# Kernel optimization log

Measured on AMD Instinct MI355X. Metric: run time of the kernel, lower is better.

The kernel has to match this reference:

```python
import jax, jax.numpy as jnp
import numpy as np

H, DH = 16, 64            # heads, dim_head (rope dim == DH)
NUM_CHAINS = 2
TWO_PI = 2.0 * np.pi
LN_EPS = 1e-5


def layer_norm(x, gamma):
    mu = jnp.mean(x, axis=-1, keepdims=True)
    var = jnp.var(x, axis=-1, keepdims=True)
    return (x - mu) * jax.lax.rsqrt(var + LN_EPS) * gamma


def rotate_half(x):
    # pairs are interleaved: (..., d*2) viewed as (..., d, 2); (x1,x2)->(-x2,x1)
    x1 = x[..., 0::2]
    x2 = x[..., 1::2]
    return jnp.stack((-x2, x1), axis=-1).reshape(x.shape)


def cyclic_rope_freqs(residue_index, chain_index, cyclic_mask, rope_freqs, dtype):
    """Angles [B,L,DH]: standard RoPE (with chain-offset combination) for linear
    tokens, ring harmonics omega_i = 2*pi*k_i/L_chain for cyclic tokens."""
    t = residue_index.astype(dtype)                      # B L (interpolate_factor=1)
    ci = chain_index.astype(dtype)
    F = rope_freqs.shape[0]                              # DH//2 = 32
    # standard path (RotaryEmbedding._forward with chain_index):
    # residue_indices = arange(F)%F = identity; chain_indices = arange(F)//F = 0
    res = t[..., None] * rope_freqs                      # B L F
    ch0 = ci * rope_freqs[0]                             # B L  (chain_freqs[...,0])
    std = jnp.repeat(res + ch0[..., None], 2, axis=-1)   # B L DH (interleaved repeat)
    # ring size per token: count of cyclic tokens on each token's chain
    oh = jax.nn.one_hot(chain_index, NUM_CHAINS, dtype=dtype)        # B L C
    counts = jnp.einsum('blc,bl->bc', oh, cyclic_mask)               # B C
    ring = jnp.take_along_axis(counts, chain_index, axis=1) * cyclic_mask  # B L
    ring_safe = jnp.maximum(ring, 1.0)
    max_k = jnp.maximum(jnp.floor(ring_safe * 0.5), 1.0)             # B L
    kk = jnp.arange(1, F + 1, dtype=dtype)
    k_eff = jnp.where(max_k[..., None] == 1.0, 1.0,
                      1.0 + jnp.mod(kk - 1.0, max_k[..., None]))     # B L F
    omega = TWO_PI * k_eff / ring_safe[..., None]                    # B L F
    cyc = jnp.repeat(omega * t[..., None], 2, axis=-1)               # B L DH
    return jnp.where((cyclic_mask > 0)[..., None], cyc, std)


def setup_inputs() -> dict:
    key = jax.random.key(0)
    ks = jax.random.split(key, 8)
    B, L, dim = 4, 1024, 1024
    s = 0.02
    x = jax.random.normal(ks[0], (B, L, dim), jnp.float32)
    time = jax.random.normal(ks[1], (B, 1, dim), jnp.float32)
    seq_mask = jnp.ones((B, L), jnp.float32)
    residue_index = (jnp.arange(B * L, dtype=jnp.int32).reshape(B, L)) % L
    chain_index = jax.random.randint(ks[2], (B, L), 0, NUM_CHAINS).astype(jnp.int32)
    cyclic_mask = jax.random.randint(ks[3], (B, L), 0, 2).astype(jnp.float32)
    gamma = jnp.ones((dim,), jnp.float32)
    Wt = jax.random.normal(ks[4], (2 * dim, dim), jnp.float32) * s
    bt = jnp.zeros((2 * dim,), jnp.float32)
    Wq = jax.random.normal(ks[5], (H * DH, dim), jnp.float32) * s
    Wkv = jax.random.normal(ks[6], (2 * H * DH, dim), jnp.float32) * s
    Wo = jax.random.normal(ks[7], (dim, H * DH), jnp.float32) * s
    rope_freqs = 1.0 / (10000.0 ** (jnp.arange(0, DH, 2, dtype=jnp.float32) / DH))
    return {"x": x, "time": time, "seq_mask": seq_mask, "cyclic_mask": cyclic_mask,
            "gamma": gamma, "Wt": Wt, "bt": bt, "Wq": Wq, "Wkv": Wkv, "Wo": Wo,
            "rope_freqs": rope_freqs,
            "residue_index": residue_index, "chain_index": chain_index}


def reference(x, time, seq_mask, cyclic_mask, gamma, Wt, bt, Wq, Wkv, Wo,
              rope_freqs, residue_index, chain_index):
    B, L, dim = x.shape
    x = x * seq_mask[..., None]
    xn = layer_norm(x, gamma)
    # time conditioning: SiLU -> Linear -> (scale, shift)
    ss = jax.nn.silu(time) @ Wt.T + bt                   # B 1 2*dim
    scale, shift = jnp.split(ss, 2, axis=-1)
    xc = xn * (scale + 1.0) + shift                      # B L dim
    q = (xc @ Wq.T).reshape(B, L, H, DH).transpose(0, 2, 1, 3)   # B H L Dh
    k, v = jnp.split(xc @ Wkv.T, 2, axis=-1)
    k = k.reshape(B, L, H, DH).transpose(0, 2, 1, 3)
    v = v.reshape(B, L, H, DH).transpose(0, 2, 1, 3)
    # cyclic rotary embeddings (full head dim rotated)
    freqs = cyclic_rope_freqs(residue_index, chain_index, cyclic_mask,
                              rope_freqs, x.dtype)        # B L DH
    cos_f = jnp.cos(freqs)[:, None]                       # B 1 L DH
    sin_f = jnp.sin(freqs)[:, None]
    q = q * cos_f + rotate_half(q) * sin_f
    k = k * cos_f + rotate_half(k) * sin_f
    sim = jnp.einsum('bhid,bhjd->bhij', q * (DH ** -0.5), k)
    neg = -jnp.finfo(sim.dtype).max
    sim = jnp.where(seq_mask[:, None, None, :] > 0, sim, neg)
    attn = jax.nn.softmax(sim, axis=-1)
    out = jnp.einsum('bhij,bhjd->bhid', attn, v)
    out = out.transpose(0, 2, 1, 3).reshape(B, L, H * DH)
    out = out @ Wo.T
    return out * seq_mask[..., None]
```

## Files before the change

kernel.cpp:

```cpp
#include <hip/hip_runtime.h>
#include <math.h>

#define NB 4
#define NL 1024
#define NDIM 1024
#define NH 16
#define NDH 64
#define NEG_MAX (-3.402823466e38f)

typedef __attribute__((ext_vector_type(4))) float fx4;
typedef __attribute__((ext_vector_type(8))) short bh8;

__device__ __forceinline__ ushort f2bf(float f){
    unsigned u = __float_as_uint(f);
    u += 0x7fff + ((u>>16)&1);
    return (ushort)(u>>16);
}
__device__ __forceinline__ float bf2f(ushort h){
    return __uint_as_float(((unsigned)h)<<16);
}
__device__ __forceinline__ void gload16(const void* g, void* l){
    __builtin_amdgcn_global_load_lds((const __attribute__((address_space(1))) void*)g,
                                     (__attribute__((address_space(3))) void*)l, 16, 0, 0);
}

__global__ __launch_bounds__(256) void k_silu(const float* __restrict__ t, float* __restrict__ o){
    int i = blockIdx.x*256 + threadIdx.x;
    float v = t[i];
    o[i] = v / (1.f + __expf(-v));
}

__global__ __launch_bounds__(256) void k_ss(const float* __restrict__ st, const float* __restrict__ Wt,
                                            const float* __restrict__ bt, float* __restrict__ ss){
    int gw   = (blockIdx.x*256 + threadIdx.x) >> 6;
    int lane = threadIdx.x & 63;
    int b = gw >> 11, j = gw & 2047;
    const float* a = st + b*NDIM;
    const float* w = Wt + (size_t)j*NDIM;
    float s = 0.f;
    #pragma unroll 4
    for (int i = lane; i < NDIM; i += 64) s += a[i]*w[i];
    #pragma unroll
    for (int off=32; off; off>>=1) s += __shfl_xor(s, off, 64);
    if (!lane) ss[gw] = s + bt[j];
}

__global__ __launch_bounds__(256) void k_counts(const int* __restrict__ chain, const float* __restrict__ cyc,
                                                float* __restrict__ counts){
    int b = blockIdx.x >> 1, c = blockIdx.x & 1;
    float s = 0.f;
    for (int l = threadIdx.x; l < NL; l += 256)
        s += (chain[b*NL+l]==c) ? cyc[b*NL+l] : 0.f;
    __shared__ float red[4];
    #pragma unroll
    for (int off=32; off; off>>=1) s += __shfl_xor(s, off, 64);
    if (!(threadIdx.x & 63)) red[threadIdx.x>>6] = s;
    __syncthreads();
    if (!threadIdx.x) counts[blockIdx.x] = red[0]+red[1]+red[2]+red[3];
}

__global__ __launch_bounds__(256) void k_angles(const int* __restrict__ resi, const int* __restrict__ chain,
                                                const float* __restrict__ cyc, const float* __restrict__ rf,
                                                const float* __restrict__ counts,
                                                float* __restrict__ cosb, float* __restrict__ sinb){
    int idx = blockIdx.x*256 + threadIdx.x;
    int f  = idx & 31;
    int bl = idx >> 5;
    int b  = bl >> 10;
    float t  = (float)resi[bl];
    int   ci = chain[bl];
    float cm = cyc[bl];
    float ang;
    if (cm > 0.f) {
        float ring      = counts[b*2+ci] * cm;
        float ring_safe = fmaxf(ring, 1.f);
        float max_k     = fmaxf(floorf(ring_safe*0.5f), 1.f);
        float k_eff     = (max_k == 1.f) ? 1.f : (1.f + fmodf((float)f, max_k));
        float omega     = 6.28318530717958647692f * k_eff / ring_safe;
        ang = omega * t;
    } else {
        ang = t * rf[f] + (float)ci * rf[0];
    }
    cosb[idx] = cosf(ang);
    sinb[idx] = sinf(ang);
}

__global__ __launch_bounds__(256) void k_conv(const float* __restrict__ s, ushort* __restrict__ d){
    int i = (blockIdx.x*256 + threadIdx.x)*4;
    fx4 v = *(const fx4*)(s+i);
    ushort4 o; o.x=f2bf(v.x); o.y=f2bf(v.y); o.z=f2bf(v.z); o.w=f2bf(v.w);
    *(ushort4*)(d+i) = o;
}

__global__ __launch_bounds__(256) void k_lnmod(const float* __restrict__ x, const float* __restrict__ sm,
                                               const float* __restrict__ gamma, const float* __restrict__ ss,
                                               ushort* __restrict__ xc){
    int row = blockIdx.x;
    int b   = row >> 10;
    int t   = threadIdx.x;
    float msk = sm[row];
    fx4 v = ((const fx4*)(x + (size_t)row*NDIM))[t];
    v.x*=msk; v.y*=msk; v.z*=msk; v.w*=msk;
    float s1 = v.x+v.y+v.z+v.w;
    float s2 = v.x*v.x + v.y*v.y + v.z*v.z + v.w*v.w;
    __shared__ float r1[4], r2[4];
    #pragma unroll
    for (int off=32; off; off>>=1){ s1 += __shfl_xor(s1,off,64); s2 += __shfl_xor(s2,off,64); }
    if (!(t & 63)){ r1[t>>6]=s1; r2[t>>6]=s2; }
    __syncthreads();
    s1 = r1[0]+r1[1]+r1[2]+r1[3];
    s2 = r2[0]+r2[1]+r2[2]+r2[3];
    float mu  = s1 * (1.f/NDIM);
    float var = s2 * (1.f/NDIM) - mu*mu;
    float rs  = rsqrtf(var + 1e-5f);
    const float* sc = ss + b*2048;
    fx4 g   = ((const fx4*)gamma)[t];
    fx4 scl = ((const fx4*)sc)[t];
    fx4 sh  = ((const fx4*)(sc+1024))[t];
    ushort4 ob;
    ob.x = f2bf((v.x-mu)*rs*g.x*(1.f+scl.x)+sh.x);
    ob.y = f2bf((v.y-mu)*rs*g.y*(1.f+scl.y)+sh.y);
    ob.z = f2bf((v.z-mu)*rs*g.z*(1.f+scl.z)+sh.z);
    ob.w = f2bf((v.w-mu)*rs*g.w*(1.f+scl.w)+sh.w);
    *(ushort4*)(xc + (size_t)row*NDIM + t*4) = ob;
}

template<int MODE>
__global__ __launch_bounds__(256) void k_mm(const ushort* __restrict__ A, const ushort* __restrict__ W,
                                            ushort* __restrict__ qo, ushort* __restrict__ ko,
                                            ushort* __restrict__ vo,
                                            float* __restrict__ outf, const float* __restrict__ smask){
    __shared__ ushort As[128*32];
    __shared__ ushort Bs[128*32];
    int t = threadIdx.x, l = t&63, w = t>>6;
    int lo = l&15, hi = l>>4;
    int m0 = blockIdx.y*128, n0 = blockIdx.x*128;
    int wm = (w>>1)*64, wn = (w&1)*64;
    fx4 acc[4][4];
    #pragma unroll
    for (int i=0;i<4;i++)
        #pragma unroll
        for (int j=0;j<4;j++) acc[i][j] = (fx4){0.f,0.f,0.f,0.f};
    const char* Ab = (const char*)A;
    const char* Wb = (const char*)W;
    for (int k0=0; k0<NDIM; k0+=32){
        __syncthreads();
        #pragma unroll
        for (int e=0;e<2;e++){
            int c = t + e*256;
            int row = c>>2, cw = c&3;
            gload16(Ab + (size_t)(m0+row)*2048 + k0*2 + cw*16, (char*)As + c*16);
            gload16(Wb + (size_t)(n0+row)*2048 + k0*2 + cw*16, (char*)Bs + c*16);
        }
        __syncthreads();
        bh8 af[4], bf[4];
        #pragma unroll
        for (int i=0;i<4;i++) af[i] = *(const bh8*)(As + (wm + i*16 + lo)*32 + hi*8);
        #pragma unroll
        for (int j=0;j<4;j++) bf[j] = *(const bh8*)(Bs + (wn + j*16 + lo)*32 + hi*8);
        #pragma unroll
        for (int i=0;i<4;i++)
            #pragma unroll
            for (int j=0;j<4;j++)
                acc[i][j] = __builtin_amdgcn_mfma_f32_16x16x32_bf16(af[i], bf[j], acc[i][j], 0, 0, 0);
    }
    #pragma unroll
    for (int i=0;i<4;i++){
        #pragma unroll
        for (int r=0;r<4;r++){
            int m = m0 + wm + i*16 + hi*4 + r;
            int b_ = m>>10, l_ = m&1023;
            #pragma unroll
            for (int j=0;j<4;j++){
                int n = n0 + wn + j*16 + lo;
                float val = acc[i][j][r];
                if (MODE==0){
                    int nn = n & 1023;
                    int h_ = nn>>6, d_ = nn&63;
                    size_t off = (size_t)((b_*NH + h_)*NL + l_)*NDH + d_;
                    if (n < 1024)      qo[off] = f2bf(val);
                    else if (n < 2048) ko[off] = f2bf(val);
                    else               vo[off] = f2bf(val);
                } else {
                    outf[(size_t)m*NDIM + n] = val * smask[m];
                }
            }
        }
    }
}

__global__ __launch_bounds__(256) void k_rope(ushort* __restrict__ q, ushort* __restrict__ k,
                                              const float* __restrict__ cosb, const float* __restrict__ sinb){
    int idx = blockIdx.x*256 + threadIdx.x;
    int f   = idx & 31;
    int bhl = idx >> 5;
    int l   = bhl & 1023;
    int b   = bhl >> 14;
    int ca  = ((b<<10)|l)*32 + f;
    float c = cosb[ca], s = sinb[ca];
    unsigned qp = ((const unsigned*)q)[idx];
    unsigned kp = ((const unsigned*)k)[idx];
    float qx = bf2f((ushort)(qp&0xffffu)), qy = bf2f((ushort)(qp>>16));
    float kx = bf2f((ushort)(kp&0xffffu)), ky = bf2f((ushort)(kp>>16));
    float q0 = (qx*c - qy*s)*0.125f, q1 = (qy*c + qx*s)*0.125f;
    float k0 = kx*c - ky*s,          k1 = ky*c + kx*s;
    ((unsigned*)q)[idx] = (unsigned)f2bf(q0) | ((unsigned)f2bf(q1)<<16);
    ((unsigned*)k)[idx] = (unsigned)f2bf(k0) | ((unsigned)f2bf(k1)<<16);
}

__global__ __launch_bounds__(256) void k_vt(const ushort* __restrict__ v, ushort* __restrict__ vt){
    __shared__ ushort tile[64][65];
    int t = threadIdx.x;
    int bh = blockIdx.y, l0 = blockIdx.x*64;
    #pragma unroll
    for (int e=0;e<2;e++){
        int c = t + e*256;
        int row = c>>3, cw = c&7;
        bh8 d = *(const bh8*)(v + ((size_t)bh*NL + l0 + row)*NDH + cw*8);
        #pragma unroll
        for (int x=0;x<8;x++) tile[row][cw*8+x] = (ushort)d[x];
    }
    __syncthreads();
    #pragma unroll
    for (int e=0;e<2;e++){
        int c = t + e*256;
        int drow = c>>3, cw = c&7;
        bh8 o;
        #pragma unroll
        for (int x=0;x<8;x++) o[x] = (short)tile[cw*8+x][drow];
        *(bh8*)(vt + ((size_t)bh*NDH + drow)*NL + l0 + cw*8) = o;
    }
}

__global__ __launch_bounds__(256) void k_fattn(const ushort* __restrict__ qb, const ushort* __restrict__ kb,
                                               const ushort* __restrict__ vt, const float* __restrict__ smask,
                                               ushort* __restrict__ ao){
    __shared__ ushort Ks[64*64];
    __shared__ ushort Vs[64*64];
    __shared__ ushort Ps[4][16*64];
    __shared__ float  smt[64];
    int t = threadIdx.x, l = t&63, w = t>>6;
    int bh = blockIdx.y, b = bh>>4, h = bh&15;
    int q0 = blockIdx.x*64;
    int lo = l&15, hi = l>>4;

    const ushort* qrowp = qb + ((size_t)bh*NL + q0 + w*16 + lo)*NDH;
    bh8 aq0 = *(const bh8*)(qrowp + hi*8);
    bh8 aq1 = *(const bh8*)(qrowp + 32 + hi*8);

    fx4 o[4];
    float mrun[4], lrun[4];
    #pragma unroll
    for (int d=0;d<4;d++) o[d] = (fx4){0.f,0.f,0.f,0.f};
    #pragma unroll
    for (int r=0;r<4;r++){ mrun[r]=NEG_MAX; lrun[r]=0.f; }

    const char* kbase = (const char*)(kb + (size_t)bh*NL*NDH);
    const char* vbase = (const char*)(vt + (size_t)bh*NDH*NL);
    char* KsB = (char*)Ks;
    char* VsB = (char*)Vs;
    char* PsB = (char*)&Ps[w][0];

    for (int j0=0; j0<NL; j0+=64){
        __syncthreads();
        #pragma unroll
        for (int e=0;e<2;e++){
            int c = t + e*256;
            int row = c>>3, cw = c&7;
            int lc = cw ^ (row&7);
            gload16(kbase + (size_t)(j0+row)*128 + lc*16, KsB + c*16);
            gload16(vbase + (size_t)row*2048 + j0*2 + lc*16, VsB + c*16);
        }
        if (t < 64) smt[t] = smask[b*NL + j0 + t];
        __syncthreads();

        fx4 s[4];
        #pragma unroll
        for (int j=0;j<4;j++){
            int row = j*16 + lo;
            int swz = (row&7)<<4;
            bh8 bk0 = *(const bh8*)(KsB + row*128 + ((hi*16) ^ swz));
            bh8 bk1 = *(const bh8*)(KsB + row*128 + ((64 + hi*16) ^ swz));
            fx4 z = (fx4){0.f,0.f,0.f,0.f};
            z = __builtin_amdgcn_mfma_f32_16x16x32_bf16(aq0, bk0, z, 0,0,0);
            z = __builtin_amdgcn_mfma_f32_16x16x32_bf16(aq1, bk1, z, 0,0,0);
            float msk = smt[row];
            s[j] = (msk > 0.f) ? z : (fx4){NEG_MAX,NEG_MAX,NEG_MAX,NEG_MAX};
        }

        float p[4][4];
        #pragma unroll
        for (int r=0;r<4;r++){
            float mt = fmaxf(fmaxf(s[0][r],s[1][r]), fmaxf(s[2][r],s[3][r]));
            #pragma unroll
            for (int off=1; off<16; off<<=1) mt = fmaxf(mt, __shfl_xor(mt, off));
            float mnew = fmaxf(mrun[r], mt);
            float cc = __expf(mrun[r]-mnew);
            float rs = 0.f;
            #pragma unroll
            for (int j=0;j<4;j++){ p[j][r] = __expf(s[j][r]-mnew); rs += p[j][r]; }
            #pragma unroll
            for (int off=1; off<16; off<<=1) rs += __shfl_xor(rs, off);
            lrun[r] = lrun[r]*cc + rs;
            mrun[r] = mnew;
            #pragma unroll
            for (int d=0;d<4;d++) o[d][r] *= cc;
        }

        #pragma unroll
        for (int r=0;r<4;r++){
            int qr = hi*4 + r;
            int swz = (qr&7)<<4;
            #pragma unroll
            for (int j=0;j<4;j++){
                int kv = j*16 + lo;
                *(ushort*)(PsB + qr*128 + ((kv*2) ^ swz)) = f2bf(p[j][r]);
            }
        }
        int swq = (lo&7)<<4;
        bh8 ap0 = *(const bh8*)(PsB + lo*128 + ((hi*16) ^ swq));
        bh8 ap1 = *(const bh8*)(PsB + lo*128 + ((64 + hi*16) ^ swq));

        #pragma unroll
        for (int d=0;d<4;d++){
            int row = d*16 + lo;
            int swz = (row&7)<<4;
            bh8 bv0 = *(const bh8*)(VsB + row*128 + ((hi*16) ^ swz));
            bh8 bv1 = *(const bh8*)(VsB + row*128 + ((64 + hi*16) ^ swz));
            o[d] = __builtin_amdgcn_mfma_f32_16x16x32_bf16(ap0, bv0, o[d], 0,0,0);
            o[d] = __builtin_amdgcn_mfma_f32_16x16x32_bf16(ap1, bv1, o[d], 0,0,0);
        }
    }

    #pragma unroll
    for (int r=0;r<4;r++){
        float inv = 1.f / lrun[r];
        int l_ = q0 + w*16 + hi*4 + r;
        size_t base = ((size_t)b*NL + l_)*NDIM + h*NDH;
        #pragma unroll
        for (int d=0;d<4;d++)
            ao[base + d*16 + lo] = f2bf(o[d][r]*inv);
    }
}

extern "C" void kernel_launch(void* const* d_in, const int* in_sizes, int n_in,
                              void* d_out, int out_size, void* d_ws, size_t ws_size,
                              hipStream_t stream) {
    const float* x      = (const float*)d_in[0];
    const float* time_  = (const float*)d_in[1];
    const float* smask  = (const float*)d_in[2];
    const float* cycm   = (const float*)d_in[3];
    const float* gamma  = (const float*)d_in[4];
    const float* Wt     = (const float*)d_in[5];
    const float* bt     = (const float*)d_in[6];
    const float* Wq     = (const float*)d_in[7];
    const float* Wkv    = (const float*)d_in[8];
    const float* Wo     = (const float*)d_in[9];
    const float* rf     = (const float*)d_in[10];
    const int*   resi   = (const int*)d_in[11];
    const int*   chain  = (const int*)d_in[12];
    float* out = (float*)d_out;

    float*  silu_t = (float*)d_ws;
    float*  ss     = silu_t + 4096;
    float*  cnts   = ss + 8192;
    float*  cosb   = cnts + 16;
    float*  sinb   = cosb + 131072;
    ushort* xc     = (ushort*)(sinb + 131072);
    ushort* wqkv   = xc + 4194304;
    ushort* wo     = wqkv + 3145728;
    ushort* qbuf   = wo + 1048576;
    ushort* kbuf   = qbuf + 4194304;
    ushort* vbuf   = kbuf + 4194304;
    ushort* vtb    = vbuf + 4194304;
    ushort* aob    = vtb + 4194304;

    hipLaunchKernelGGL(k_silu,   dim3(16),        dim3(256), 0, stream, time_, silu_t);
    hipLaunchKernelGGL(k_ss,     dim3(2048),      dim3(256), 0, stream, silu_t, Wt, bt, ss);
    hipLaunchKernelGGL(k_counts, dim3(8),         dim3(256), 0, stream, chain, cycm, cnts);
    hipLaunchKernelGGL(k_angles, dim3(512),       dim3(256), 0, stream, resi, chain, cycm, rf, cnts, cosb, sinb);
    hipLaunchKernelGGL(k_conv,   dim3(1024),      dim3(256), 0, stream, Wq,  wqkv);
    hipLaunchKernelGGL(k_conv,   dim3(2048),      dim3(256), 0, stream, Wkv, wqkv + 1048576);
    hipLaunchKernelGGL(k_conv,   dim3(1024),      dim3(256), 0, stream, Wo,  wo);
    hipLaunchKernelGGL(k_lnmod,  dim3(4096),      dim3(256), 0, stream, x, smask, gamma, ss, xc);
    hipLaunchKernelGGL((k_mm<0>), dim3(24,32),    dim3(256), 0, stream, xc, wqkv, qbuf, kbuf, vbuf, (float*)nullptr, (const float*)nullptr);
    hipLaunchKernelGGL(k_rope,   dim3(8192),      dim3(256), 0, stream, qbuf, kbuf, cosb, sinb);
    hipLaunchKernelGGL(k_vt,     dim3(16,64),     dim3(256), 0, stream, vbuf, vtb);
    hipLaunchKernelGGL(k_fattn,  dim3(16,64),     dim3(256), 0, stream, qbuf, kbuf, vtb, smask, aob);
    hipLaunchKernelGGL((k_mm<1>), dim3(8,32),     dim3(256), 0, stream, aob, wo, (ushort*)nullptr, (ushort*)nullptr, (ushort*)nullptr, out, smask);
}
```

Measured before the change: 250.2 us.

## Restructure flash attention with double-buffered KV, 128-row tiles and exp2 softmax

```diff
diff --git a/kernel.cpp b/kernel.cpp
--- a/kernel.cpp
+++ b/kernel.cpp
@@ -1,4 +1,5 @@
 #include <hip/hip_runtime.h>
+#include <hip/hip_bf16.h>
 #include <math.h>
 
 #define NB 4
@@ -12,9 +13,8 @@
 typedef __attribute__((ext_vector_type(8))) short bh8;
 
 __device__ __forceinline__ ushort f2bf(float f){
-    unsigned u = __float_as_uint(f);
-    u += 0x7fff + ((u>>16)&1);
-    return (ushort)(u>>16);
+    __hip_bfloat16 h = __float2bfloat16(f);
+    return *(ushort*)&h;
 }
 __device__ __forceinline__ float bf2f(ushort h){
     return __uint_as_float(((unsigned)h)<<16);
@@ -24,22 +24,19 @@
                                      (__attribute__((address_space(3))) void*)l, 16, 0, 0);
 }
 
-__global__ __launch_bounds__(256) void k_silu(const float* __restrict__ t, float* __restrict__ o){
-    int i = blockIdx.x*256 + threadIdx.x;
-    float v = t[i];
-    o[i] = v / (1.f + __expf(-v));
-}
-
-__global__ __launch_bounds__(256) void k_ss(const float* __restrict__ st, const float* __restrict__ Wt,
+__global__ __launch_bounds__(256) void k_ss(const float* __restrict__ time_, const float* __restrict__ Wt,
                                             const float* __restrict__ bt, float* __restrict__ ss){
     int gw   = (blockIdx.x*256 + threadIdx.x) >> 6;
     int lane = threadIdx.x & 63;
     int b = gw >> 11, j = gw & 2047;
-    const float* a = st + b*NDIM;
+    const float* a = time_ + b*NDIM;
     const float* w = Wt + (size_t)j*NDIM;
     float s = 0.f;
     #pragma unroll 4
-    for (int i = lane; i < NDIM; i += 64) s += a[i]*w[i];
+    for (int i = lane; i < NDIM; i += 64){
+        float v = a[i];
+        s += (v / (1.f + __expf(-v))) * w[i];
+    }
     #pragma unroll
     for (int off=32; off; off>>=1) s += __shfl_xor(s, off, 64);
     if (!lane) ss[gw] = s + bt[j];
@@ -85,11 +82,22 @@
     sinb[idx] = sinf(ang);
 }
 
-__global__ __launch_bounds__(256) void k_conv(const float* __restrict__ s, ushort* __restrict__ d){
+__global__ __launch_bounds__(256) void k_convall(const float* __restrict__ Wq, const float* __restrict__ Wkv,
+                                                 const float* __restrict__ Wo,
+                                                 ushort* __restrict__ wqkv, ushort* __restrict__ wo){
     int i = (blockIdx.x*256 + threadIdx.x)*4;
-    fx4 v = *(const fx4*)(s+i);
+    if (i >= 4194304) return;
+    const float* src; ushort* dst;
+    if (i < 3145728){
+        dst = wqkv + i;
+        src = (i < 1048576) ? (Wq + i) : (Wkv + (i - 1048576));
+    } else {
+        dst = wo + (i - 3145728);
+        src = Wo + (i - 3145728);
+    }
+    fx4 v = *(const fx4*)src;
     ushort4 o; o.x=f2bf(v.x); o.y=f2bf(v.y); o.z=f2bf(v.z); o.w=f2bf(v.w);
-    *(ushort4*)(d+i) = o;
+    *(ushort4*)dst = o;
 }
 
 __global__ __launch_bounds__(256) void k_lnmod(const float* __restrict__ x, const float* __restrict__ sm,
@@ -198,12 +206,13 @@
     int b   = bhl >> 14;
     int ca  = ((b<<10)|l)*32 + f;
     float c = cosb[ca], s = sinb[ca];
+    const float QS = 0.18033688011112042f;
     unsigned qp = ((const unsigned*)q)[idx];
     unsigned kp = ((const unsigned*)k)[idx];
     float qx = bf2f((ushort)(qp&0xffffu)), qy = bf2f((ushort)(qp>>16));
     float kx = bf2f((ushort)(kp&0xffffu)), ky = bf2f((ushort)(kp>>16));
-    float q0 = (qx*c - qy*s)*0.125f, q1 = (qy*c + qx*s)*0.125f;
-    float k0 = kx*c - ky*s,          k1 = ky*c + kx*s;
+    float q0 = (qx*c - qy*s)*QS, q1 = (qy*c + qx*s)*QS;
+    float k0 = kx*c - ky*s,      k1 = ky*c + kx*s;
     ((unsigned*)q)[idx] = (unsigned)f2bf(q0) | ((unsigned)f2bf(q1)<<16);
     ((unsigned*)k)[idx] = (unsigned)f2bf(k0) | ((unsigned)f2bf(k1)<<16);
 }
@@ -235,111 +244,164 @@
 __global__ __launch_bounds__(256) void k_fattn(const ushort* __restrict__ qb, const ushort* __restrict__ kb,
                                                const ushort* __restrict__ vt, const float* __restrict__ smask,
                                                ushort* __restrict__ ao){
-    __shared__ ushort Ks[64*64];
-    __shared__ ushort Vs[64*64];
-    __shared__ ushort Ps[4][16*64];
-    __shared__ float  smt[64];
+    __shared__ ushort Ks[2][64*64];
+    __shared__ ushort Vs[2][64*64];
+    __shared__ ushort Ps[4][32*64];
     int t = threadIdx.x, l = t&63, w = t>>6;
-    int bh = blockIdx.y, b = bh>>4, h = bh&15;
-    int q0 = blockIdx.x*64;
     int lo = l&15, hi = l>>4;
-
-    const ushort* qrowp = qb + ((size_t)bh*NL + q0 + w*16 + lo)*NDH;
-    bh8 aq0 = *(const bh8*)(qrowp + hi*8);
-    bh8 aq1 = *(const bh8*)(qrowp + 32 + hi*8);
-
-    fx4 o[4];
-    float mrun[4], lrun[4];
-    #pragma unroll
-    for (int d=0;d<4;d++) o[d] = (fx4){0.f,0.f,0.f,0.f};
-    #pragma unroll
-    for (int r=0;r<4;r++){ mrun[r]=NEG_MAX; lrun[r]=0.f; }
+    int logical = (blockIdx.x & 7)*64 + (blockIdx.x >> 3);
+    int bh = logical >> 3;
+    int qt = logical & 7;
+    int b = bh>>4, h = bh&15;
+    int q0 = qt*128;
+    int swzq = (lo&7)<<4;
+
+    bh8 aq[2][2];
+    #pragma unroll
+    for (int qs=0; qs<2; qs++){
+        const ushort* qrow = qb + ((size_t)bh*NL + q0 + w*32 + qs*16 + lo)*NDH;
+        aq[qs][0] = *(const bh8*)(qrow + hi*8);
+        aq[qs][1] = *(const bh8*)(qrow + 32 + hi*8);
+    }
+    const float* mrow = smask + b*NL;
+
+    fx4 o[2][4];
+    float mrun[2], lrun[2];
+    #pragma unroll
+    for (int qs=0; qs<2; qs++){
+        mrun[qs]=NEG_MAX; lrun[qs]=0.f;
+        #pragma unroll
+        for (int dt=0; dt<4; dt++) o[qs][dt] = (fx4){0.f,0.f,0.f,0.f};
+    }
 
     const char* kbase = (const char*)(kb + (size_t)bh*NL*NDH);
     const char* vbase = (const char*)(vt + (size_t)bh*NDH*NL);
-    char* KsB = (char*)Ks;
-    char* VsB = (char*)Vs;
-    char* PsB = (char*)&Ps[w][0];
-
-    for (int j0=0; j0<NL; j0+=64){
-        __syncthreads();
-        #pragma unroll
-        for (int e=0;e<2;e++){
-            int c = t + e*256;
-            int row = c>>3, cw = c&7;
-            int lc = cw ^ (row&7);
-            gload16(kbase + (size_t)(j0+row)*128 + lc*16, KsB + c*16);
-            gload16(vbase + (size_t)row*2048 + j0*2 + lc*16, VsB + c*16);
-        }
-        if (t < 64) smt[t] = smask[b*NL + j0 + t];
-        __syncthreads();
-
-        fx4 s[4];
+
+    #define STAGE(bb, jt) { \
+        int j0s = (jt)*64; \
+        _Pragma("unroll") \
+        for (int e=0;e<2;e++){ \
+            int c = t + e*256; \
+            int row = c>>3, cw = c&7; \
+            int lc = cw ^ (row&7); \
+            gload16(kbase + (size_t)(j0s+row)*128 + lc*16, (char*)Ks[bb] + c*16); \
+        } \
+        _Pragma("unroll") \
+        for (int e=0;e<2;e++){ \
+            int c = t + e*256; \
+            int row = c>>3, cw = c&7; \
+            int lc = cw ^ (row&7); \
+            gload16(vbase + (size_t)row*2048 + j0s*2 + lc*16, (char*)Vs[bb] + c*16); \
+        } }
+
+    STAGE(0, 0);
+    __syncthreads();
+
+    for (int tt=0; tt<16; ++tt){
+        int cur = tt & 1;
+        if (tt < 15) STAGE(cur^1, tt+1);
+        int j0 = tt*64;
+        const char* KsB = (const char*)Ks[cur];
+        const char* VsB = (const char*)Vs[cur];
+        char* PsB = (char*)&Ps[w][0];
+
+        bh8 kf[4][2];
         #pragma unroll
         for (int j=0;j<4;j++){
             int row = j*16 + lo;
             int swz = (row&7)<<4;
-            bh8 bk0 = *(const bh8*)(KsB + row*128 + ((hi*16) ^ swz));
-            bh8 bk1 = *(const bh8*)(KsB + row*128 + ((64 + hi*16) ^ swz));
-            fx4 z = (fx4){0.f,0.f,0.f,0.f};
-            z = __builtin_amdgcn_mfma_f32_16x16x32_bf16(aq0, bk0, z, 0,0,0);
-            z = __builtin_amdgcn_mfma_f32_16x16x32_bf16(aq1, bk1, z, 0,0,0);
-            float msk = smt[row];
-            s[j] = (msk > 0.f) ? z : (fx4){NEG_MAX,NEG_MAX,NEG_MAX,NEG_MAX};
-        }
-
-        float p[4][4];
-        #pragma unroll
-        for (int r=0;r<4;r++){
-            float mt = fmaxf(fmaxf(s[0][r],s[1][r]), fmaxf(s[2][r],s[3][r]));
-            #pragma unroll
-            for (int off=1; off<16; off<<=1) mt = fmaxf(mt, __shfl_xor(mt, off));
-            float mnew = fmaxf(mrun[r], mt);
-            float cc = __expf(mrun[r]-mnew);
+            kf[j][0] = *(const bh8*)(KsB + row*128 + ((hi*16) ^ swz));
+            kf[j][1] = *(const bh8*)(KsB + row*128 + ((64 + hi*16) ^ swz));
+        }
+        fx4 s[2][4];
+        #pragma unroll
+        for (int qs=0; qs<2; qs++)
+            #pragma unroll
+            for (int j=0;j<4;j++){
+                fx4 z = (fx4){0.f,0.f,0.f,0.f};
+                z = __builtin_amdgcn_mfma_f32_16x16x32_bf16(kf[j][0], aq[qs][0], z, 0,0,0);
+                z = __builtin_amdgcn_mfma_f32_16x16x32_bf16(kf[j][1], aq[qs][1], z, 0,0,0);
+                s[qs][j] = z;
+            }
+        #pragma unroll
+        for (int j=0;j<4;j++){
+            float4 mv = *(const float4*)(mrow + j0 + j*16 + hi*4);
+            s[0][j][0] = mv.x>0.f ? s[0][j][0] : NEG_MAX;  s[1][j][0] = mv.x>0.f ? s[1][j][0] : NEG_MAX;
+            s[0][j][1] = mv.y>0.f ? s[0][j][1] : NEG_MAX;  s[1][j][1] = mv.y>0.f ? s[1][j][1] : NEG_MAX;
+            s[0][j][2] = mv.z>0.f ? s[0][j][2] : NEG_MAX;  s[1][j][2] = mv.z>0.f ? s[1][j][2] : NEG_MAX;
+            s[0][j][3] = mv.w>0.f ? s[0][j][3] : NEG_MAX;  s[1][j][3] = mv.w>0.f ? s[1][j][3] : NEG_MAX;
+        }
+
+        #pragma unroll
+        for (int qs=0; qs<2; qs++){
+            float mt = s[qs][0][0];
+            #pragma unroll
+            for (int j=0;j<4;j++)
+                #pragma unroll
+                for (int r=0;r<4;r++) mt = fmaxf(mt, s[qs][j][r]);
+            mt = fmaxf(mt, __shfl_xor(mt, 16));
+            mt = fmaxf(mt, __shfl_xor(mt, 32));
+            float mnew = fmaxf(mrun[qs], mt);
+            float cc = __builtin_amdgcn_exp2f(mrun[qs] - mnew);
+            float p[4][4];
             float rs = 0.f;
             #pragma unroll
-            for (int j=0;j<4;j++){ p[j][r] = __expf(s[j][r]-mnew); rs += p[j][r]; }
-            #pragma unroll
-            for (int off=1; off<16; off<<=1) rs += __shfl_xor(rs, off);
-            lrun[r] = lrun[r]*cc + rs;
-            mrun[r] = mnew;
-            #pragma unroll
-            for (int d=0;d<4;d++) o[d][r] *= cc;
-        }
-
-        #pragma unroll
-        for (int r=0;r<4;r++){
-            int qr = hi*4 + r;
-            int swz = (qr&7)<<4;
-            #pragma unroll
-            for (int j=0;j<4;j++){
-                int kv = j*16 + lo;
-                *(ushort*)(PsB + qr*128 + ((kv*2) ^ swz)) = f2bf(p[j][r]);
+            for (int j=0;j<4;j++)
+                #pragma unroll
+                for (int r=0;r<4;r++){ p[j][r] = __builtin_amdgcn_exp2f(s[qs][j][r] - mnew); rs += p[j][r]; }
+            rs += __shfl_xor(rs, 16);
+            rs += __shfl_xor(rs, 32);
+            lrun[qs] = lrun[qs]*cc + rs;
+            mrun[qs] = mnew;
+            #pragma unroll
+            for (int r=0;r<4;r++){
+                float ccr = __shfl(cc, hi*4 + r);
+                #pragma unroll
+                for (int dt=0; dt<4; dt++) o[qs][dt][r] *= ccr;
             }
-        }
-        int swq = (lo&7)<<4;
-        bh8 ap0 = *(const bh8*)(PsB + lo*128 + ((hi*16) ^ swq));
-        bh8 ap1 = *(const bh8*)(PsB + lo*128 + ((64 + hi*16) ^ swq));
-
-        #pragma unroll
-        for (int d=0;d<4;d++){
-            int row = d*16 + lo;
+            #pragma unroll
+            for (int j=0;j<4;j++)
+                #pragma unroll
+                for (int pp=0; pp<2; pp++){
+                    unsigned word = (unsigned)f2bf(p[j][2*pp]) | ((unsigned)f2bf(p[j][2*pp+1])<<16);
+                    int kv0 = j*16 + hi*4 + 2*pp;
+                    *(unsigned*)(PsB + (qs*16+lo)*128 + ((kv0*2) ^ swzq)) = word;
+                }
+        }
+
+        bh8 ap[2][2];
+        #pragma unroll
+        for (int qs=0; qs<2; qs++){
+            ap[qs][0] = *(const bh8*)(PsB + (qs*16+lo)*128 + ((hi*16) ^ swzq));
+            ap[qs][1] = *(const bh8*)(PsB + (qs*16+lo)*128 + ((64 + hi*16) ^ swzq));
+        }
+        #pragma unroll
+        for (int dt=0; dt<4; dt++){
+            int row = dt*16 + lo;
             int swz = (row&7)<<4;
             bh8 bv0 = *(const bh8*)(VsB + row*128 + ((hi*16) ^ swz));
             bh8 bv1 = *(const bh8*)(VsB + row*128 + ((64 + hi*16) ^ swz));
-            o[d] = __builtin_amdgcn_mfma_f32_16x16x32_bf16(ap0, bv0, o[d], 0,0,0);
-            o[d] = __builtin_amdgcn_mfma_f32_16x16x32_bf16(ap1, bv1, o[d], 0,0,0);
-        }
-    }
-
-    #pragma unroll
-    for (int r=0;r<4;r++){
-        float inv = 1.f / lrun[r];
-        int l_ = q0 + w*16 + hi*4 + r;
-        size_t base = ((size_t)b*NL + l_)*NDIM + h*NDH;
-        #pragma unroll
-        for (int d=0;d<4;d++)
-            ao[base + d*16 + lo] = f2bf(o[d][r]*inv);
+            o[0][dt] = __builtin_amdgcn_mfma_f32_16x16x32_bf16(ap[0][0], bv0, o[0][dt], 0,0,0);
+            o[0][dt] = __builtin_amdgcn_mfma_f32_16x16x32_bf16(ap[0][1], bv1, o[0][dt], 0,0,0);
+            o[1][dt] = __builtin_amdgcn_mfma_f32_16x16x32_bf16(ap[1][0], bv0, o[1][dt], 0,0,0);
+            o[1][dt] = __builtin_amdgcn_mfma_f32_16x16x32_bf16(ap[1][1], bv1, o[1][dt], 0,0,0);
+        }
+        __syncthreads();
+    }
+    #undef STAGE
+
+    #pragma unroll
+    for (int qs=0; qs<2; qs++){
+        float inv = 1.f / lrun[qs];
+        #pragma unroll
+        for (int r=0;r<4;r++){
+            float ivr = __shfl(inv, hi*4 + r);
+            int l_ = q0 + w*32 + qs*16 + hi*4 + r;
+            size_t base = ((size_t)b*NL + l_)*NDIM + h*NDH;
+            #pragma unroll
+            for (int dt=0; dt<4; dt++)
+                ao[base + dt*16 + lo] = f2bf(o[qs][dt][r] * ivr);
+        }
     }
 }
 
@@ -361,8 +423,7 @@
     const int*   chain  = (const int*)d_in[12];
     float* out = (float*)d_out;
 
-    float*  silu_t = (float*)d_ws;
-    float*  ss     = silu_t + 4096;
+    float*  ss     = (float*)d_ws;
     float*  cnts   = ss + 8192;
     float*  cosb   = cnts + 16;
     float*  sinb   = cosb + 131072;
@@ -375,17 +436,14 @@
     ushort* vtb    = vbuf + 4194304;
     ushort* aob    = vtb + 4194304;
 
-    hipLaunchKernelGGL(k_silu,   dim3(16),        dim3(256), 0, stream, time_, silu_t);
-    hipLaunchKernelGGL(k_ss,     dim3(2048),      dim3(256), 0, stream, silu_t, Wt, bt, ss);
-    hipLaunchKernelGGL(k_counts, dim3(8),         dim3(256), 0, stream, chain, cycm, cnts);
-    hipLaunchKernelGGL(k_angles, dim3(512),       dim3(256), 0, stream, resi, chain, cycm, rf, cnts, cosb, sinb);
-    hipLaunchKernelGGL(k_conv,   dim3(1024),      dim3(256), 0, stream, Wq,  wqkv);
-    hipLaunchKernelGGL(k_conv,   dim3(2048),      dim3(256), 0, stream, Wkv, wqkv + 1048576);
-    hipLaunchKernelGGL(k_conv,   dim3(1024),      dim3(256), 0, stream, Wo,  wo);
-    hipLaunchKernelGGL(k_lnmod,  dim3(4096),      dim3(256), 0, stream, x, smask, gamma, ss, xc);
-    hipLaunchKernelGGL((k_mm<0>), dim3(24,32),    dim3(256), 0, stream, xc, wqkv, qbuf, kbuf, vbuf, (float*)nullptr, (const float*)nullptr);
-    hipLaunchKernelGGL(k_rope,   dim3(8192),      dim3(256), 0, stream, qbuf, kbuf, cosb, sinb);
-    hipLaunchKernelGGL(k_vt,     dim3(16,64),     dim3(256), 0, stream, vbuf, vtb);
-    hipLaunchKernelGGL(k_fattn,  dim3(16,64),     dim3(256), 0, stream, qbuf, kbuf, vtb, smask, aob);
-    hipLaunchKernelGGL((k_mm<1>), dim3(8,32),     dim3(256), 0, stream, aob, wo, (ushort*)nullptr, (ushort*)nullptr, (ushort*)nullptr, out, smask);
-}
+    hipLaunchKernelGGL(k_ss,      dim3(2048),    dim3(256), 0, stream, time_, Wt, bt, ss);
+    hipLaunchKernelGGL(k_counts,  dim3(8),       dim3(256), 0, stream, chain, cycm, cnts);
+    hipLaunchKernelGGL(k_angles,  dim3(512),     dim3(256), 0, stream, resi, chain, cycm, rf, cnts, cosb, sinb);
+    hipLaunchKernelGGL(k_convall, dim3(4096),    dim3(256), 0, stream, Wq, Wkv, Wo, wqkv, wo);
+    hipLaunchKernelGGL(k_lnmod,   dim3(4096),    dim3(256), 0, stream, x, smask, gamma, ss, xc);
+    hipLaunchKernelGGL((k_mm<0>), dim3(24,32),   dim3(256), 0, stream, xc, wqkv, qbuf, kbuf, vbuf, (float*)nullptr, (const float*)nullptr);
+    hipLaunchKernelGGL(k_rope,    dim3(8192),    dim3(256), 0, stream, qbuf, kbuf, cosb, sinb);
+    hipLaunchKernelGGL(k_vt,      dim3(16,64),   dim3(256), 0, stream, vbuf, vtb);
+    hipLaunchKernelGGL(k_fattn,   dim3(512),     dim3(256), 0, stream, qbuf, kbuf, vtb, smask, aob);
+    hipLaunchKernelGGL((k_mm<1>), dim3(8,32),    dim3(256), 0, stream, aob, wo, (ushort*)nullptr, (ushort*)nullptr, (ushort*)nullptr, out, smask);
+}
```

Result: faster. 230.7 us (-7.8%).
